# Kernel tuning notes

Hardware: AMD Instinct MI355X
Metric: run time of the kernel (lower is better)

Reference implementation:

```python
import jax, jax.numpy as jnp
import numpy as np

HD_DIM = 4096
BUNDLE_SIZE = 128
STRIDE = 128  # bundle_size - overlap, overlap = 0
EPS = 1e-8


def setup_inputs() -> dict:
    key = jax.random.key(0)
    k1, k2 = jax.random.split(key)
    inputs = jax.random.normal(k1, (4, 2048, HD_DIM), dtype=jnp.float32)
    # base vector ~ N(0, 1/sqrt(hd_dim)) as in RandomNormal(stddev=1/sqrt(hd_dim))
    base = jax.random.normal(k2, (HD_DIM,), dtype=jnp.float32) / jnp.sqrt(jnp.float32(HD_DIM))
    # position_weights initialized to decay_rate**i
    pos_w = jnp.power(jnp.float32(0.99), jnp.arange(BUNDLE_SIZE, dtype=jnp.float32))
    return {"inputs": inputs, "bundle_position_base": base, "position_weights": pos_w}


def reference(inputs, bundle_position_base, position_weights):
    B, S, D = inputs.shape
    nb = (S - BUNDLE_SIZE) // STRIDE + 1  # number of bundles

    # Cyclic-shift position vectors: pos[s, d] = base[(d - s) mod D]
    shifts = jnp.arange(BUNDLE_SIZE)
    idx = jnp.mod(jnp.arange(D)[None, :] - shifts[:, None], D)  # [bs, D]
    pos = bundle_position_base[idx]                              # [bs, D]
    w = jax.nn.softmax(position_weights)                         # [bs]
    pos = pos * w[:, None]

    # overlap=0 and S divisible by bundle_size -> bundles tile the sequence
    tok = inputs.reshape(B, nb, BUNDLE_SIZE, D)  # [B, nb, bs, D]

    # circular correlation: real(ifft(fft(tok) * conj(fft(pos))))
    # both operands real -> use rfft/irfft (identical math, half the work)
    tok_f = jnp.fft.rfft(tok, axis=-1)                 # [B, nb, bs, D//2+1]
    pos_f = jnp.conj(jnp.fft.rfft(pos, axis=-1))       # [bs, D//2+1]
    bound = jnp.fft.irfft(tok_f * pos_f[None, None], n=D, axis=-1)  # [B, nb, bs, D]

    bundle = jnp.sum(bound, axis=2)  # [B, nb, D]
    # tf.nn.l2_normalize: x * rsqrt(max(sum(x^2), eps))
    ssq = jnp.sum(bundle * bundle, axis=-1, keepdims=True)
    return (bundle * jax.lax.rsqrt(jnp.maximum(ssq, EPS))).astype(jnp.float32)
```

## Files before the change

### kernel.cpp

```cpp
#include <hip/hip_runtime.h>

#define D 4096
#define DM (D - 1)
#define BS 128
#define NROW 64
#define QC 8
#define JC 8

__device__ __forceinline__ float4 ldswz(const float* bsh, int G) {
  const int pg = G ^ ((G >> 3) & 7);
  return *(const float4*)(bsh + (pg << 2));
}

__global__ __launch_bounds__(256) void shift_k(const float* __restrict__ tok,
                                               const float* __restrict__ pw,
                                               float* __restrict__ part) {
  const int t = threadIdx.x;
  const int qc = blockIdx.x;
  const int row = blockIdx.y;

  __shared__ float wsh[BS];
  __shared__ float red[4];
  {
    const float v = (t < BS) ? pw[t] : -1e30f;
    float m = v;
#pragma unroll
    for (int o = 32; o > 0; o >>= 1) m = fmaxf(m, __shfl_xor(m, o));
    if ((t & 63) == 0) red[t >> 6] = m;
    __syncthreads();
    m = fmaxf(fmaxf(red[0], red[1]), fmaxf(red[2], red[3]));
    const float e = (t < BS) ? expf(v - m) : 0.f;
    float s = e;
#pragma unroll
    for (int o = 32; o > 0; o >>= 1) s += __shfl_xor(s, o);
    __syncthreads();
    if ((t & 63) == 0) red[t >> 6] = s;
    __syncthreads();
    s = red[0] + red[1] + red[2] + red[3];
    if (t < BS) wsh[t] = e / s;
    __syncthreads();
  }
  float wv[16];
#pragma unroll
  for (int j = 0; j < 16; ++j) wv[j] = wsh[(qc << 4) + j];

  const float4* tr = (const float4*)(tok + (size_t)row * (BS * D));
  float4 acc[4];
#pragma unroll
  for (int g = 0; g < 4; ++g) acc[g] = make_float4(0.f, 0.f, 0.f, 0.f);

#pragma unroll
  for (int qq = 0; qq < 4; ++qq) {
    const int q = (qc << 2) + qq;
    const float w0 = wv[4 * qq + 0], w1 = wv[4 * qq + 1];
    const float w2 = wv[4 * qq + 2], w3 = wv[4 * qq + 3];
#pragma unroll
    for (int g = 0; g < 4; ++g) {
      const int G = (t + (g << 8) + q) & 1023;
      const int G1 = (G + 1) & 1023;
      const size_t r0 = (size_t)(4 * q + 0) << 10;
      const size_t r1 = (size_t)(4 * q + 1) << 10;
      const size_t r2 = (size_t)(4 * q + 2) << 10;
      const size_t r3 = (size_t)(4 * q + 3) << 10;
      const float4 a0 = tr[r0 + G];
      const float4 a1 = tr[r1 + G], b1 = tr[r1 + G1];
      const float4 a2 = tr[r2 + G], b2 = tr[r2 + G1];
      const float4 a3 = tr[r3 + G], b3 = tr[r3 + G1];
      acc[g].x += w0 * a0.x; acc[g].y += w0 * a0.y;
      acc[g].z += w0 * a0.z; acc[g].w += w0 * a0.w;
      acc[g].x += w1 * a1.y; acc[g].y += w1 * a1.z;
      acc[g].z += w1 * a1.w; acc[g].w += w1 * b1.x;
      acc[g].x += w2 * a2.z; acc[g].y += w2 * a2.w;
      acc[g].z += w2 * b2.x; acc[g].w += w2 * b2.y;
      acc[g].x += w3 * a3.w; acc[g].y += w3 * b3.x;
      acc[g].z += w3 * b3.y; acc[g].w += w3 * b3.z;
    }
  }
  float4* pz = (float4*)(part + (size_t)(qc * NROW + row) * D);
#pragma unroll
  for (int g = 0; g < 4; ++g) pz[t + (g << 8)] = acc[g];
}

__global__ __launch_bounds__(256) void corr_k(const float* __restrict__ part,
                                              const float* __restrict__ base,
                                              float* __restrict__ braw) {
  __shared__ __align__(16) float zsh[512];
  __shared__ __align__(16) float bsh[4608];
  const int t = threadIdx.x;
  const int jc = blockIdx.x;
  const int row = blockIdx.y;
  const int jb = jc << 9;

#pragma unroll
  for (int i = 0; i < 2; ++i) {
    const int ml = t + (i << 8);
    const int mg = jb + ml;
    float s = 0.f;
#pragma unroll
    for (int cc = 0; cc < QC; ++cc)
      s += part[(size_t)(cc * NROW + row) * D + mg];
    zsh[ml] = s;
  }
  for (int x = t; x < 4608; x += 256) {
    const int g = x >> 2;
    const int pg = g ^ ((g >> 3) & 7);
    bsh[(pg << 2) | (x & 3)] = base[(x + jb) & DM];
  }
  __syncthreads();

  const int Gb = 1024 - 4 * t;
  float acc[16];
#pragma unroll
  for (int k = 0; k < 16; ++k) acc[k] = 0.f;

  float4 win[8];
  win[4] = ldswz(bsh, Gb - 4);
  win[5] = ldswz(bsh, Gb - 3);
  win[6] = ldswz(bsh, Gb - 2);
  win[7] = ldswz(bsh, Gb - 1);

  const float4* zsh4 = (const float4*)zsh;
  for (int io = 0; io < 16; ++io) {
#pragma unroll
    for (int ic = 0; ic < 8; ++ic) {
      const int i = (io << 3) + ic;
      win[ic] = ldswz(bsh, Gb + i);
      const float4 zv = zsh4[i];
      const float4 u0 = win[(ic + 4) & 7];
      const float4 u1 = win[(ic + 5) & 7];
      const float4 u2 = win[(ic + 6) & 7];
      const float4 u3 = win[(ic + 7) & 7];
      const float4 u4 = win[ic];
      const float wf[20] = {u0.x, u0.y, u0.z, u0.w, u1.x, u1.y, u1.z, u1.w,
                            u2.x, u2.y, u2.z, u2.w, u3.x, u3.y, u3.z, u3.w,
                            u4.x, u4.y, u4.z, u4.w};
      const float zz[4] = {zv.x, zv.y, zv.z, zv.w};
#pragma unroll
      for (int k = 0; k < 16; ++k) {
#pragma unroll
        for (int jj = 0; jj < 4; ++jj)
          acc[k] += zz[jj] * wf[16 + jj - k];
      }
    }
  }
  float4* op4 = (float4*)(braw + (size_t)(jc * NROW + row) * D + (t << 4));
  op4[0] = make_float4(acc[0], acc[1], acc[2], acc[3]);
  op4[1] = make_float4(acc[4], acc[5], acc[6], acc[7]);
  op4[2] = make_float4(acc[8], acc[9], acc[10], acc[11]);
  op4[3] = make_float4(acc[12], acc[13], acc[14], acc[15]);
}

__global__ __launch_bounds__(1024) void norm_k(const float* __restrict__ braw,
                                               float* __restrict__ out) {
  const int t = threadIdx.x;
  const int row = blockIdx.x;
  const float4* b4 = (const float4*)braw;
  float4 s = make_float4(0.f, 0.f, 0.f, 0.f);
#pragma unroll
  for (int p = 0; p < JC; ++p) {
    const float4 v = b4[(size_t)(p * NROW + row) * (D / 4) + t];
    s.x += v.x; s.y += v.y; s.z += v.z; s.w += v.w;
  }
  float ssq = s.x * s.x + s.y * s.y + s.z * s.z + s.w * s.w;
#pragma unroll
  for (int o = 32; o > 0; o >>= 1) ssq += __shfl_xor(ssq, o);
  __shared__ float red[16];
  if ((t & 63) == 0) red[t >> 6] = ssq;
  __syncthreads();
  float tot = 0.f;
#pragma unroll
  for (int i = 0; i < 16; ++i) tot += red[i];
  const float sc = rsqrtf(fmaxf(tot, 1e-8f));
  float4 o;
  o.x = s.x * sc; o.y = s.y * sc; o.z = s.z * sc; o.w = s.w * sc;
  ((float4*)out)[(size_t)row * (D / 4) + t] = o;
}

extern "C" void kernel_launch(void* const* d_in, const int* in_sizes, int n_in,
                              void* d_out, int out_size, void* d_ws, size_t ws_size,
                              hipStream_t stream) {
  (void)in_sizes; (void)n_in; (void)out_size; (void)ws_size;
  const float* tok = (const float*)d_in[0];
  const float* base = (const float*)d_in[1];
  const float* pw = (const float*)d_in[2];
  float* out = (float*)d_out;

  float* part = (float*)d_ws;
  float* braw = part + (size_t)QC * NROW * D;

  shift_k<<<dim3(QC, NROW), 256, 0, stream>>>(tok, pw, part);
  corr_k<<<dim3(JC, NROW), 256, 0, stream>>>(part, base, braw);
  norm_k<<<NROW, 1024, 0, stream>>>(braw, out);
}
```

Baseline: 228.4 us.

## Recast circular correlation as bf16 MFMA matmul with separate z reduction kernel

The partial-sum reduction moves into a new z_k kernel that writes the reduced rows as bf16. The FP32 scalar sliding-window correlation in corr_k is replaced by a Toeplitz-style matrix multiply on 16x16x32 bf16 MFMA instructions, with shared-memory tiles of bf16 z values and shifted base vectors. The aim is to move the correlation's FMA work onto matrix cores. This lowers precision to bf16 for both operands, adds a kernel launch, and launches more, smaller blocks.

Result: faster. 208.5 us (-8.7%).

```diff
diff --git a/kernel.cpp b/kernel.cpp
--- a/kernel.cpp
+++ b/kernel.cpp
@@ -1,15 +1,23 @@
 #include <hip/hip_runtime.h>
 
 #define D 4096
-#define DM (D - 1)
+#define DM 4095
 #define BS 128
 #define NROW 64
 #define QC 8
 #define JC 8
 
-__device__ __forceinline__ float4 ldswz(const float* bsh, int G) {
-  const int pg = G ^ ((G >> 3) & 7);
-  return *(const float4*)(bsh + (pg << 2));
+#define ZSTR 520
+#define PSTR 616
+
+typedef __attribute__((ext_vector_type(8))) short bf16x8;
+typedef __attribute__((ext_vector_type(4))) float f32x4;
+
+__device__ __forceinline__ unsigned short f2bf(float f) {
+  union { float f; unsigned int u; } v;
+  v.f = f;
+  const unsigned int r = v.u + 0x7fffu + ((v.u >> 16) & 1u);
+  return (unsigned short)(r >> 16);
 }
 
 __global__ __launch_bounds__(256) void shift_k(const float* __restrict__ tok,
@@ -81,73 +89,77 @@
   for (int g = 0; g < 4; ++g) pz[t + (g << 8)] = acc[g];
 }
 
-__global__ __launch_bounds__(256) void corr_k(const float* __restrict__ part,
+__global__ __launch_bounds__(256) void z_k(const float* __restrict__ part,
+                                           unsigned short* __restrict__ zb) {
+  const int t = threadIdx.x;
+  const int mq = blockIdx.x;
+  const int row = blockIdx.y;
+  const int m0 = (mq << 10) + (t << 2);
+  float4 s = make_float4(0.f, 0.f, 0.f, 0.f);
+#pragma unroll
+  for (int cc = 0; cc < QC; ++cc) {
+    const float4 v = *(const float4*)(part + (size_t)(cc * NROW + row) * D + m0);
+    s.x += v.x; s.y += v.y; s.z += v.z; s.w += v.w;
+  }
+  ushort4 o;
+  o.x = f2bf(s.x); o.y = f2bf(s.y); o.z = f2bf(s.z); o.w = f2bf(s.w);
+  *(ushort4*)(zb + (size_t)row * D + m0) = o;
+}
+
+__global__ __launch_bounds__(256) void corr_k(const unsigned short* __restrict__ zb,
                                               const float* __restrict__ base,
                                               float* __restrict__ braw) {
-  __shared__ __align__(16) float zsh[512];
-  __shared__ __align__(16) float bsh[4608];
+  __shared__ __align__(16) unsigned short zsh[16 * ZSTR];
+  __shared__ __align__(16) unsigned short psh[8 * PSTR];
   const int t = threadIdx.x;
   const int jc = blockIdx.x;
-  const int row = blockIdx.y;
+  const int dg = blockIdx.y;
+  const int rt = blockIdx.z;
   const int jb = jc << 9;
-
-#pragma unroll
-  for (int i = 0; i < 2; ++i) {
-    const int ml = t + (i << 8);
-    const int mg = jb + ml;
-    float s = 0.f;
-#pragma unroll
-    for (int cc = 0; cc < QC; ++cc)
-      s += part[(size_t)(cc * NROW + row) * D + mg];
-    zsh[ml] = s;
-  }
-  for (int x = t; x < 4608; x += 256) {
-    const int g = x >> 2;
-    const int pg = g ^ ((g >> 3) & 7);
-    bsh[(pg << 2) | (x & 3)] = base[(x + jb) & DM];
+  const int d0b = dg << 6;
+
+  {
+    const int rr = t >> 4;
+    const int c0 = (t & 15) << 5;
+    const uint4* src =
+        (const uint4*)(zb + (size_t)(rt * 16 + rr) * D + jb + c0);
+    uint4* dst = (uint4*)(zsh + rr * ZSTR + c0);
+    dst[0] = src[0];
+    dst[1] = src[1];
+    dst[2] = src[2];
+    dst[3] = src[3];
+  }
+  {
+    const int c0 = jb - d0b - 64 + 2 * D;
+    for (int idx = t; idx < 8 * PSTR; idx += 256) {
+      const int r = idx / PSTR;
+      const int x = idx - r * PSTR;
+      psh[idx] = f2bf(base[(c0 + r + x) & DM]);
+    }
   }
   __syncthreads();
 
-  const int Gb = 1024 - 4 * t;
-  float acc[16];
-#pragma unroll
-  for (int k = 0; k < 16; ++k) acc[k] = 0.f;
-
-  float4 win[8];
-  win[4] = ldswz(bsh, Gb - 4);
-  win[5] = ldswz(bsh, Gb - 3);
-  win[6] = ldswz(bsh, Gb - 2);
-  win[7] = ldswz(bsh, Gb - 1);
-
-  const float4* zsh4 = (const float4*)zsh;
-  for (int io = 0; io < 16; ++io) {
-#pragma unroll
-    for (int ic = 0; ic < 8; ++ic) {
-      const int i = (io << 3) + ic;
-      win[ic] = ldswz(bsh, Gb + i);
-      const float4 zv = zsh4[i];
-      const float4 u0 = win[(ic + 4) & 7];
-      const float4 u1 = win[(ic + 5) & 7];
-      const float4 u2 = win[(ic + 6) & 7];
-      const float4 u3 = win[(ic + 7) & 7];
-      const float4 u4 = win[ic];
-      const float wf[20] = {u0.x, u0.y, u0.z, u0.w, u1.x, u1.y, u1.z, u1.w,
-                            u2.x, u2.y, u2.z, u2.w, u3.x, u3.y, u3.z, u3.w,
-                            u4.x, u4.y, u4.z, u4.w};
-      const float zz[4] = {zv.x, zv.y, zv.z, zv.w};
-#pragma unroll
-      for (int k = 0; k < 16; ++k) {
-#pragma unroll
-        for (int jj = 0; jj < 4; ++jj)
-          acc[k] += zz[jj] * wf[16 + jj - k];
-      }
-    }
-  }
-  float4* op4 = (float4*)(braw + (size_t)(jc * NROW + row) * D + (t << 4));
-  op4[0] = make_float4(acc[0], acc[1], acc[2], acc[3]);
-  op4[1] = make_float4(acc[4], acc[5], acc[6], acc[7]);
-  op4[2] = make_float4(acc[8], acc[9], acc[10], acc[11]);
-  op4[3] = make_float4(acc[12], acc[13], acc[14], acc[15]);
+  const int lane = t & 63;
+  const int w = t >> 6;
+  const int dd = lane & 15;
+  const int q = lane >> 4;
+  const int a0 = 64 + (q << 3) - (w << 4) - dd;
+  const int pr = a0 & 7;
+  const int px = a0 - pr;
+  const unsigned short* pA = psh + pr * PSTR + px;
+  const unsigned short* pB = zsh + dd * ZSTR + (q << 3);
+
+  f32x4 acc = {0.f, 0.f, 0.f, 0.f};
+#pragma unroll
+  for (int ks = 0; ks < 16; ++ks) {
+    const bf16x8 af = *(const bf16x8*)(pA + (ks << 5));
+    const bf16x8 bf = *(const bf16x8*)(pB + (ks << 5));
+    acc = __builtin_amdgcn_mfma_f32_16x16x32_bf16(af, bf, acc, 0, 0, 0);
+  }
+  const int row = rt * 16 + dd;
+  const int d = d0b + (w << 4) + (q << 2);
+  float4 o = make_float4(acc[0], acc[1], acc[2], acc[3]);
+  *(float4*)(braw + (size_t)(jc * NROW + row) * D + d) = o;
 }
 
 __global__ __launch_bounds__(1024) void norm_k(const float* __restrict__ braw,
@@ -187,8 +199,11 @@
 
   float* part = (float*)d_ws;
   float* braw = part + (size_t)QC * NROW * D;
+  unsigned short* zb =
+      (unsigned short*)(braw + (size_t)JC * NROW * D);
 
   shift_k<<<dim3(QC, NROW), 256, 0, stream>>>(tok, pw, part);
-  corr_k<<<dim3(JC, NROW), 256, 0, stream>>>(part, base, braw);
+  z_k<<<dim3(4, NROW), 256, 0, stream>>>(part, zb);
+  corr_k<<<dim3(JC, 64, 4), 256, 0, stream>>>(zb, base, braw);
   norm_k<<<NROW, 1024, 0, stream>>>(braw, out);
 }
```
